# Kernel tuning notes

Hardware: AMD Instinct MI355X
Metric: run time of the kernel (lower is better)

Reference implementation:

```python
import jax, jax.numpy as jnp
import numpy as np

EPS = 1e-4
IN_DIM, D1, D2 = 30, 20, 15


def _orthogonal(key, rows, cols):
    # mimic nn.init.orthogonal_ for a (rows, cols) matrix with rows < cols
    a = jax.random.normal(key, (cols, rows), dtype=jnp.float32)
    q, _ = jnp.linalg.qr(a)  # (cols, rows) with orthonormal columns
    return q.T  # (rows, cols), rows orthonormal


def setup_inputs() -> dict:
    key = jax.random.key(0)
    kx, k1, k2 = jax.random.split(key, 3)
    X = jax.random.normal(kx, (65536, IN_DIM, IN_DIM), dtype=jnp.float32)
    W1 = _orthogonal(k1, D1, IN_DIM)
    W2 = _orthogonal(k2, D2, D1)
    return {"X": X, "W1": W1, "W2": W2}


def _bimap(X, W):
    # W @ X @ W^T, symmetrized, + eps*I  -> (b, out, out)
    Y = jnp.einsum('oi,bij,pj->bop', W, X, W)
    Y = (Y + jnp.swapaxes(Y, -1, -2)) * 0.5
    return Y + EPS * jnp.eye(W.shape[0], dtype=Y.dtype)


def _reeig(X):
    w, v = jnp.linalg.eigh(X)
    w = jnp.maximum(w, EPS)
    return jnp.einsum('bik,bk,bjk->bij', v, w, v)


def _logeig(X):
    w, v = jnp.linalg.eigh(X)
    w = jnp.log(jnp.maximum(w, EPS))
    return jnp.einsum('bik,bk,bjk->bij', v, w, v)


def reference(X, W1, W2):
    X = _reeig(_bimap(X, W1))            # (b, 20, 20)
    X = _logeig(_reeig(_bimap(X, W2)))   # (b, 15, 15)
    iu0, iu1 = jnp.triu_indices(D2)      # row-major upper-tri, matches torch.triu_indices
    return X[:, iu0, iu1]                # (b, 120)
```

## Files before the change

### kernel.cpp

```cpp
#include <hip/hip_runtime.h>

#define EPSV 1e-4f

__device__ __forceinline__ float bperm(int addr4, float v) {
  return __int_as_float(__builtin_amdgcn_ds_bpermute(addr4, __float_as_int(v)));
}

__device__ __forceinline__ void wave_fence() { asm volatile("" ::: "memory"); }

template<int N>
__device__ __forceinline__ float selN(const float (&a)[N], int idx) {
  float r = a[0];
#pragma unroll
  for (int k = 1; k < N; ++k) r = (idx == k) ? a[k] : r;
  return r;
}

template<int N>
__device__ void jacobi_eig(float (&a)[N], float (&v)[N], int l, int base4,
                           bool laneValid, float tolsq, int maxSweeps)
{
  constexpr int NH = N / 2;
  const int partner = N - 1 - l;
  const int pslot = (l < NH) ? l : partner;
  const int qslot = N - 1 - pslot;
  const int p4 = base4 + 4 * pslot;
  const int q4 = base4 + 4 * qslot;
  const int pr4 = base4 + 4 * partner;
  const int srcl = (l == 0) ? 0 : ((l == 1) ? (N - 1) : (l - 1));
  const int src4 = base4 + 4 * srcl;
  const bool isP = (l < NH);

  float dval = selN<N>(a, l);
  int sweep = 0;
  while (true) {
    float offAcc = 0.0f;
    for (int r = 0; r < N - 1; ++r) {
      float anti = selN<N>(a, partner);
      float app = bperm(p4, dval);
      float aqq = bperm(q4, dval);
      float apq = bperm(p4, anti);

      float absq = fabsf(apq);
      bool ok = absq > 1e-28f;
      float apqs = ok ? apq : 1.0f;
      float theta = 0.5f * (aqq - app) / apqs;
      float tt = 1.0f / (fabsf(theta) + sqrtf(theta * theta + 1.0f));
      tt = (theta < 0.0f) ? -tt : tt;
      tt = ok ? tt : 0.0f;
      float c = __builtin_amdgcn_rsqf(tt * tt + 1.0f);
      float s = tt * c;
      offAcc += laneValid ? apq * apq : 0.0f;

      float seff = isP ? -s : s;
#pragma unroll
      for (int k = 0; k < N; ++k) {
        float pc = bperm(pr4, a[k]);
        a[k] = c * a[k] + seff * pc;
      }
#pragma unroll
      for (int i = 0; i < NH; ++i) {
        float ti = bperm(base4 + 4 * i, tt);
        float ci = __builtin_amdgcn_rsqf(ti * ti + 1.0f);
        float si = ti * ci;
        float x = a[i], y = a[N - 1 - i];
        a[i]         = ci * x - si * y;
        a[N - 1 - i] = si * x + ci * y;
        float xv = v[i], yv = v[N - 1 - i];
        v[i]         = ci * xv - si * yv;
        v[N - 1 - i] = si * xv + ci * yv;
      }
      float dnew = isP ? (app - tt * apq) : (aqq + tt * apq);

      float tmp[N];
#pragma unroll
      for (int k = 0; k < N; ++k) tmp[k] = bperm(src4, a[k]);
      a[0] = tmp[0];
      a[1] = tmp[N - 1];
#pragma unroll
      for (int k = 2; k < N; ++k) a[k] = tmp[k - 1];
      float xl = v[N - 1];
#pragma unroll
      for (int k = N - 1; k >= 2; --k) v[k] = v[k - 1];
      v[1] = xl;
      dval = bperm(src4, dnew);
    }
    ++sweep;
#pragma unroll
    for (int m = 1; m < 64; m <<= 1) offAcc += __shfl_xor(offAcc, m);
    if (sweep >= maxSweeps || offAcc < tolsq) break;
  }
}

__global__ __launch_bounds__(256, 5)
void spdnet_kernel(const float* __restrict__ X, const float* __restrict__ W1g,
                   const float* __restrict__ W2g, float* __restrict__ out,
                   int nBatch)
{
  __shared__ __align__(16) float sS[12 * 420];

  const int tid = threadIdx.x;
  const int wave = tid >> 6;
  const int lane = tid & 63;
  const int grp = lane / 20;
  const int l = lane - grp * 20;
  const int g3 = (grp < 3) ? grp : 2;
  const bool activeG = (grp < 3);
  const int wstart = blockIdx.x * 12 + wave * 3;
  const int bm = wstart + g3;
  const bool valid = activeG && (bm < nBatch);
  const int base4 = g3 * 80;
  float* Sm = sS + (wave * 3 + g3) * 420;

  float w1r[30];
  {
    const float2* wr = (const float2*)(W1g + l * 30);
#pragma unroll
    for (int k2 = 0; k2 < 15; ++k2) {
      float2 q = wr[k2];
      w1r[2 * k2] = q.x; w1r[2 * k2 + 1] = q.y;
    }
  }

  const int bmc = (bm < nBatch) ? bm : (nBatch - 1);
  const float4* Xm = (const float4*)(X + (size_t)bmc * 900);
  float tcol[30];
#pragma unroll
  for (int r = 0; r < 30; ++r) tcol[r] = 0.0f;
#pragma unroll
  for (int q = 0; q < 225; ++q) {
    float4 x4 = Xm[q];
    tcol[(4 * q + 0) / 30] += x4.x * w1r[(4 * q + 0) % 30];
    tcol[(4 * q + 1) / 30] += x4.y * w1r[(4 * q + 1) % 30];
    tcol[(4 * q + 2) / 30] += x4.z * w1r[(4 * q + 2) % 30];
    tcol[(4 * q + 3) / 30] += x4.w * w1r[(4 * q + 3) % 30];
  }

  float z[20];
#pragma unroll
  for (int i = 0; i < 20; ++i) z[i] = 0.0f;
  {
    const float4* W14 = (const float4*)W1g;
#pragma unroll
    for (int q = 0; q < 150; ++q) {
      float4 w4 = W14[q];
      z[(4 * q + 0) / 30] += w4.x * tcol[(4 * q + 0) % 30];
      z[(4 * q + 1) / 30] += w4.y * tcol[(4 * q + 1) % 30];
      z[(4 * q + 2) / 30] += w4.z * tcol[(4 * q + 2) % 30];
      z[(4 * q + 3) / 30] += w4.w * tcol[(4 * q + 3) % 30];
    }
  }

  if (activeG) {
#pragma unroll
    for (int k = 0; k < 20; ++k) Sm[k * 21 + l] = z[k];
  }
  wave_fence();
  float a[20], v[20];
#pragma unroll
  for (int i = 0; i < 20; ++i) {
    float zt = Sm[l * 21 + i];
    a[i] = 0.5f * (z[i] + zt) + ((i == l) ? EPSV : 0.0f);
    v[i] = (i == l) ? 1.0f : 0.0f;
  }

  jacobi_eig<20>(a, v, l, base4, valid, 2.0e-9f, 12);

  float lam1 = selN<20>(a, l);
  float gs = sqrtf(fmaxf(lam1, EPSV));

  if (activeG) {
#pragma unroll
    for (int k = 0; k < 20; ++k) Sm[l * 21 + k] = v[k];
  }
  wave_fence();
  float vcol[20];
#pragma unroll
  for (int r = 0; r < 20; ++r) vcol[r] = Sm[r * 21 + l];

  float b[15];
#pragma unroll
  for (int i = 0; i < 15; ++i) b[i] = 0.0f;
  {
    const float4* W24 = (const float4*)W2g;
#pragma unroll
    for (int q = 0; q < 75; ++q) {
      float4 w4 = W24[q];
      b[(4 * q + 0) / 20] += w4.x * vcol[(4 * q + 0) % 20];
      b[(4 * q + 1) / 20] += w4.y * vcol[(4 * q + 1) % 20];
      b[(4 * q + 2) / 20] += w4.z * vcol[(4 * q + 2) % 20];
      b[(4 * q + 3) / 20] += w4.w * vcol[(4 * q + 3) % 20];
    }
  }

  wave_fence();
  float* Ut = Sm;
  if (activeG) {
#pragma unroll
    for (int i = 0; i < 15; ++i) Ut[i * 20 + l] = gs * b[i];
  }
  wave_fence();

  const int l2 = l & 15;
  float myrow[20];
  {
    const float4* mr = (const float4*)(Ut + ((l2 < 15) ? l2 : 0) * 20);
    float msk = (l2 < 15) ? 1.0f : 0.0f;
#pragma unroll
    for (int r4 = 0; r4 < 5; ++r4) {
      float4 q = mr[r4];
      myrow[4 * r4]     = q.x * msk; myrow[4 * r4 + 1] = q.y * msk;
      myrow[4 * r4 + 2] = q.z * msk; myrow[4 * r4 + 3] = q.w * msk;
    }
  }
  float a2[16], v2[16];
  a2[15] = 0.0f;
#pragma unroll
  for (int r = 0; r < 15; ++r) {
    const float4* ur = (const float4*)(Ut + r * 20);
    float acc = 0.0f;
#pragma unroll
    for (int r4 = 0; r4 < 5; ++r4) {
      float4 q = ur[r4];
      acc += q.x * myrow[4 * r4] + q.y * myrow[4 * r4 + 1] +
             q.z * myrow[4 * r4 + 2] + q.w * myrow[4 * r4 + 3];
    }
    a2[r] = acc + ((r == l2) ? EPSV : 0.0f);
  }
#pragma unroll
  for (int k = 0; k < 16; ++k) v2[k] = (k == l2) ? 1.0f : 0.0f;

  jacobi_eig<16>(a2, v2, l2, base4, valid && (l < 16), 3.0e-10f, 12);

  float lam2 = selN<16>(a2, l2);
  float h = logf(fmaxf(lam2, EPSV));

  wave_fence();
  float* Wl = Sm;
  float* hl = Sm + 400;
  if (activeG && l < 16) {
#pragma unroll
    for (int k = 0; k < 16; ++k) Wl[l2 * 20 + k] = v2[k];
    hl[l2] = h;
  }
  wave_fence();

  if (valid && l < 15) {
    float wj[15], hw[15];
#pragma unroll
    for (int k = 0; k < 15; ++k) wj[k] = Wl[l * 20 + k];
#pragma unroll
    for (int k = 0; k < 15; ++k) hw[k] = hl[k] * wj[k];
    float* og = out + (size_t)bm * 120;
#pragma unroll
    for (int i = 0; i < 15; ++i) {
      const float* wr = Wl + i * 20;
      float acc = 0.0f;
#pragma unroll
      for (int k = 0; k < 15; ++k) acc += hw[k] * wr[k];
      if (i <= l) og[15 * i - (i * (i - 1)) / 2 + (l - i)] = acc;
    }
  }
}

extern "C" void kernel_launch(void* const* d_in, const int* in_sizes, int n_in,
                              void* d_out, int out_size, void* d_ws, size_t ws_size,
                              hipStream_t stream) {
  const float* X  = (const float*)d_in[0];
  const float* W1 = (const float*)d_in[1];
  const float* W2 = (const float*)d_in[2];
  float* out = (float*)d_out;
  int nBatch = in_sizes[0] / 900;
  int nBlocks = (nBatch + 11) / 12;
  spdnet_kernel<<<nBlocks, 256, 0, stream>>>(X, W1, W2, out, nBatch);
}
```

Before: 4.840 ms.

## Stage transposed W1 in shared memory and restructure first bimap as row-streamed loop

Stages a transposed copy of W1 in shared memory once per block. The first BiMap becomes a rolled row loop: each X row is dotted with the lane's W1 row, then the scalar is scattered into z using W1 columns read from shared memory. This replaces the fully unrolled 225-float4 plus 150-float4 global-load loops and drops the 30-element tcol register array. It also rewrites the W2 product as per-output dot products and lowers the launch-bounds occupancy hint from 5 to 4. The intent is less register pressure and smaller code, at the cost of a block-wide barrier, narrower float2 X loads, and a lower occupancy target.

```diff
diff --git a/kernel.cpp b/kernel.cpp
--- a/kernel.cpp
+++ b/kernel.cpp
@@ -92,12 +92,13 @@
   }
 }
 
-__global__ __launch_bounds__(256, 5)
+__global__ __launch_bounds__(256, 4)
 void spdnet_kernel(const float* __restrict__ X, const float* __restrict__ W1g,
                    const float* __restrict__ W2g, float* __restrict__ out,
                    int nBatch)
 {
   __shared__ __align__(16) float sS[12 * 420];
+  __shared__ __align__(16) float sW1t[30 * 20];
 
   const int tid = threadIdx.x;
   const int wave = tid >> 6;
@@ -112,6 +113,11 @@
   const int base4 = g3 * 80;
   float* Sm = sS + (wave * 3 + g3) * 420;
 
+  for (int t0 = tid; t0 < 600; t0 += 256) {
+    int i = t0 / 30, r = t0 - i * 30;
+    sW1t[r * 20 + i] = W1g[t0];
+  }
+
   float w1r[30];
   {
     const float2* wr = (const float2*)(W1g + l * 30);
@@ -121,34 +127,26 @@
       w1r[2 * k2] = q.x; w1r[2 * k2 + 1] = q.y;
     }
   }
+  __syncthreads();
 
   const int bmc = (bm < nBatch) ? bm : (nBatch - 1);
-  const float4* Xm = (const float4*)(X + (size_t)bmc * 900);
-  float tcol[30];
-#pragma unroll
-  for (int r = 0; r < 30; ++r) tcol[r] = 0.0f;
-#pragma unroll
-  for (int q = 0; q < 225; ++q) {
-    float4 x4 = Xm[q];
-    tcol[(4 * q + 0) / 30] += x4.x * w1r[(4 * q + 0) % 30];
-    tcol[(4 * q + 1) / 30] += x4.y * w1r[(4 * q + 1) % 30];
-    tcol[(4 * q + 2) / 30] += x4.z * w1r[(4 * q + 2) % 30];
-    tcol[(4 * q + 3) / 30] += x4.w * w1r[(4 * q + 3) % 30];
-  }
-
+  const float* Xm = X + (size_t)bmc * 900;
   float z[20];
 #pragma unroll
   for (int i = 0; i < 20; ++i) z[i] = 0.0f;
-  {
-    const float4* W14 = (const float4*)W1g;
-#pragma unroll
-    for (int q = 0; q < 150; ++q) {
-      float4 w4 = W14[q];
-      z[(4 * q + 0) / 30] += w4.x * tcol[(4 * q + 0) % 30];
-      z[(4 * q + 1) / 30] += w4.y * tcol[(4 * q + 1) % 30];
-      z[(4 * q + 2) / 30] += w4.z * tcol[(4 * q + 2) % 30];
-      z[(4 * q + 3) / 30] += w4.w * tcol[(4 * q + 3) % 30];
-    }
+  for (int r = 0; r < 30; ++r) {
+    const float2* xr = (const float2*)(Xm + r * 30);
+    float t0 = 0.0f, t1 = 0.0f;
+#pragma unroll
+    for (int k2 = 0; k2 < 15; ++k2) {
+      float2 q = xr[k2];
+      t0 = fmaf(q.x, w1r[2 * k2], t0);
+      t1 = fmaf(q.y, w1r[2 * k2 + 1], t1);
+    }
+    float t = t0 + t1;
+    const float* wc = sW1t + r * 20;
+#pragma unroll
+    for (int i = 0; i < 20; ++i) z[i] = fmaf(wc[i], t, z[i]);
   }
 
   if (activeG) {
@@ -180,17 +178,16 @@
 
   float b[15];
 #pragma unroll
-  for (int i = 0; i < 15; ++i) b[i] = 0.0f;
-  {
-    const float4* W24 = (const float4*)W2g;
-#pragma unroll
-    for (int q = 0; q < 75; ++q) {
-      float4 w4 = W24[q];
-      b[(4 * q + 0) / 20] += w4.x * vcol[(4 * q + 0) % 20];
-      b[(4 * q + 1) / 20] += w4.y * vcol[(4 * q + 1) % 20];
-      b[(4 * q + 2) / 20] += w4.z * vcol[(4 * q + 2) % 20];
-      b[(4 * q + 3) / 20] += w4.w * vcol[(4 * q + 3) % 20];
-    }
+  for (int i = 0; i < 15; ++i) {
+    const float4* w2r = (const float4*)(W2g + i * 20);
+    float acc = 0.0f;
+#pragma unroll
+    for (int r4 = 0; r4 < 5; ++r4) {
+      float4 q = w2r[r4];
+      acc += q.x * vcol[4 * r4] + q.y * vcol[4 * r4 + 1] +
+             q.z * vcol[4 * r4 + 2] + q.w * vcol[4 * r4 + 3];
+    }
+    b[i] = acc;
   }
 
   wave_fence();
```

Result: faster. 4.578 ms (-5.4%).
